# Kernel tuning notes

Hardware: AMD Instinct MI355X
Metric: run time of the kernel (lower is better)

The kernel has to match this reference:

```python
import jax, jax.numpy as jnp
import numpy as np

N = 50000       # num nodes
E = 800000      # num edges
F_NODE = 128    # input node feature dim
F_EDGE = 32     # input edge feature dim
H = 64          # hidden dim (heads=1)
NEG_SLOPE = 0.2 # GAT leaky-relu slope


def _segment_softmax(scores, seg, num_segments):
    # numerically stable softmax over edges grouped by destination node
    m = jax.ops.segment_max(scores, seg, num_segments=num_segments)
    ex = jnp.exp(scores - m[seg])
    denom = jax.ops.segment_sum(ex, seg, num_segments=num_segments)
    return ex / (denom[seg] + 1e-16)


def _egat_conv(x, src, dst, eattr, W, We, a_src, a_dst, a_e, b):
    # PyG-style GAT layer with edge features (heads=1, no self loops).
    xp = x @ W                      # [N, H] projected nodes
    ep = eattr @ We                 # [E, H] projected edges (returned as new edge feats)
    score = (xp @ a_src)[src] + (xp @ a_dst)[dst] + ep @ a_e  # [E]
    score = jax.nn.leaky_relu(score, NEG_SLOPE)
    alpha = _segment_softmax(score, dst, N)                    # [E]
    out = jax.ops.segment_sum(alpha[:, None] * xp[src], dst, num_segments=N) + b
    return out, alpha, ep


def setup_inputs() -> dict:
    key = jax.random.key(0)
    ks = jax.random.split(key, 24)
    inp = {
        "x": jax.random.normal(ks[0], (N, F_NODE), jnp.float32),
        "edge_index": jax.random.randint(ks[1], (2, E), 0, N, jnp.int64),
        "edge_attr": jax.random.normal(ks[2], (E, F_EDGE), jnp.float32),
    }
    def glorot(k, shape):
        fan = shape[0] + shape[-1]
        return jax.random.normal(k, shape, jnp.float32) * jnp.sqrt(2.0 / fan)
    dims = [(F_NODE, F_EDGE), (H, H), (H, H)]
    i = 3
    for li, (din, dedge) in enumerate(dims, start=1):
        inp[f"W{li}"] = glorot(ks[i], (din, H)); i += 1
        inp[f"We{li}"] = glorot(ks[i], (dedge, H)); i += 1
        inp[f"as{li}"] = glorot(ks[i], (H,)); i += 1
        inp[f"ad{li}"] = glorot(ks[i], (H,)); i += 1
        inp[f"ae{li}"] = glorot(ks[i], (H,)); i += 1
        inp[f"b{li}"] = jnp.zeros((H,), jnp.float32)
    inp["Wc"] = glorot(ks[i], (H, 1)); i += 1
    inp["bc"] = jnp.zeros((1,), jnp.float32)
    return inp


def reference(x, edge_index, edge_attr,
              W1, We1, as1, ad1, ae1, b1,
              W2, We2, as2, ad2, ae2, b2,
              W3, We3, as3, ad3, ae3, b3,
              Wc, bc):
    src, dst = edge_index[0], edge_index[1]
    # layer 1 (edge feats projected F_EDGE -> H, reused as next edge_attr)
    x1, _, e1 = _egat_conv(x, src, dst, edge_attr, W1, We1, as1, ad1, ae1, b1)
    x1 = jax.nn.relu(x1)  # dropout is identity in eval mode
    # layer 2
    x2, _, e2 = _egat_conv(x1, src, dst, e1, W2, We2, as2, ad2, ae2, b2)
    x2 = jax.nn.relu(x2)
    # layer 3
    x3, _, _ = _egat_conv(x2, src, dst, e2, W3, We3, as3, ad3, ae3, b3)
    x3 = jax.nn.relu(x3)
    return x3 @ Wc + bc  # [N, 1]
```

## Files before the change

kernel.cpp:

```cpp
#include <hip/hip_runtime.h>
#include <hip/hip_fp16.h>
#include <math.h>

#define NN 50000
#define NE 800000
#define FN 128
#define FE 32
#define HD 64
#define NB 49
#define GP ((NN + 127) / 128)
#define NT (NE / 64)
#define EB2 ((NT + 7) / 8)
#define GE ((NE + 255) / 256)

typedef unsigned long long u64;
typedef unsigned short u16;

__global__ void k_vecs_zero(const float* __restrict__ We1, const float* __restrict__ We2,
                            const float* __restrict__ We3, const float* __restrict__ ae1,
                            const float* __restrict__ ae2, const float* __restrict__ ae3,
                            float* __restrict__ v123, int* __restrict__ deg) {
  const int i = blockIdx.x * blockDim.x + threadIdx.x;
  if (i < NN) deg[i] = 0;
  if (blockIdx.x != 0) return;
  __shared__ float u2[HD], u3[HD], u23[HD];
  const int t = threadIdx.x;
  if (t < HD) {
    float s2 = 0.f, s3 = 0.f;
    for (int j = 0; j < HD; ++j) {
      s2 += We2[t * HD + j] * ae2[j];
      s3 += We3[t * HD + j] * ae3[j];
    }
    u2[t] = s2; u3[t] = s3;
  }
  __syncthreads();
  if (t < HD) {
    float s23 = 0.f;
    for (int j = 0; j < HD; ++j) s23 += We2[t * HD + j] * u3[j];
    u23[t] = s23;
  }
  __syncthreads();
  if (t < FE) {
    float a = 0.f, b = 0.f, c = 0.f;
    for (int j = 0; j < HD; ++j) {
      float w = We1[t * HD + j];
      a += w * ae1[j];
      b += w * u2[j];
      c += w * u23[j];
    }
    v123[t] = a; v123[32 + t] = b; v123[64 + t] = c;
  }
}

__global__ __launch_bounds__(256) void k_mega4(
    const float* __restrict__ x, const float* __restrict__ W,
    const float* __restrict__ asv, const float* __restrict__ adv,
    __half* __restrict__ xph, float* __restrict__ ssrc, float* __restrict__ sdst,
    const int* __restrict__ srcA, const int* __restrict__ dstA,
    const float* __restrict__ eattr, const float* __restrict__ v123,
    int* __restrict__ deg, u16* __restrict__ rank, u64* __restrict__ trec) {
  const int t = threadIdx.x;
  if (blockIdx.x >= GP) {
    const int kb = blockIdx.x - GP;
    const int w = t >> 6, lane = t & 63;
    const int g = lane >> 3, q = lane & 7;
    const float4 v1q = *(const float4*)(v123 + q * 4);
    const float4 v2q = *(const float4*)(v123 + 32 + q * 4);
    const float4 v3q = *(const float4*)(v123 + 64 + q * 4);
    const int perm = 8 * q + g;
#pragma unroll
    for (int it = 0; it < 2; ++it) {
      const int tIdx = kb * 8 + w * 2 + it;
      if (tIdx < NT) {
        const int E0 = tIdx * 64;
        const int e = E0 + perm;
        const int d = dstA[e];
        const int s = srcA[e];
        const int r = atomicAdd(&deg[d], 1);
        float ra = 0.f, rb = 0.f, rc = 0.f;
#pragma unroll
        for (int k = 0; k < 8; ++k) {
          const float4 xv =
              *(const float4*)(eattr + (size_t)(E0 + 8 * k + g) * FE + q * 4);
          float a = xv.x * v1q.x + xv.y * v1q.y + xv.z * v1q.z + xv.w * v1q.w;
          float b = xv.x * v2q.x + xv.y * v2q.y + xv.z * v2q.z + xv.w * v2q.w;
          float c = xv.x * v3q.x + xv.y * v3q.y + xv.z * v3q.z + xv.w * v3q.w;
#pragma unroll
          for (int off = 1; off < 8; off <<= 1) {
            a += __shfl_xor(a, off);
            b += __shfl_xor(b, off);
            c += __shfl_xor(c, off);
          }
          if (q == k) { ra = a; rb = b; rc = c; }
        }
        trec[e] = (u64)(u16)s
                | ((u64)__half_as_ushort(__float2half_rn(ra)) << 16)
                | ((u64)__half_as_ushort(__float2half_rn(rb)) << 32)
                | ((u64)__half_as_ushort(__float2half_rn(rc)) << 48);
        rank[e] = (u16)r;
      }
    }
    return;
  }
  const int w = t >> 6, l = t & 63;
  const int g = w * 4 + (l >> 4);
  const int rr = g * 8;
  const int c0 = (l & 15) * 4;
  const int row0 = blockIdx.x * 128;

  int xoff[8];
#pragma unroll
  for (int i = 0; i < 8; ++i) {
    int gr = row0 + rr + i;
    xoff[i] = (gr < NN ? gr : NN - 1) * FN;
  }

  float acc[8][4];
#pragma unroll
  for (int i = 0; i < 8; ++i)
#pragma unroll
    for (int j = 0; j < 4; ++j) acc[i][j] = 0.f;

  for (int k = 0; k < FN; k += 4) {
    float wv[4][4];
#pragma unroll
    for (int kk = 0; kk < 4; ++kk) {
      float4 wq = *(const float4*)(W + (k + kk) * HD + c0);
      wv[kk][0] = wq.x; wv[kk][1] = wq.y; wv[kk][2] = wq.z; wv[kk][3] = wq.w;
    }
#pragma unroll
    for (int i = 0; i < 8; ++i) {
      float4 a = *(const float4*)(x + xoff[i] + k);
#pragma unroll
      for (int j = 0; j < 4; ++j)
        acc[i][j] += a.x * wv[0][j] + a.y * wv[1][j] + a.z * wv[2][j] + a.w * wv[3][j];
    }
  }

  float as4[4], ad4[4];
#pragma unroll
  for (int j = 0; j < 4; ++j) { as4[j] = asv[c0 + j]; ad4[j] = adv[c0 + j]; }
#pragma unroll
  for (int i = 0; i < 8; ++i) {
    int gr = row0 + rr + i;
    float ps = 0.f, pd = 0.f;
#pragma unroll
    for (int j = 0; j < 4; ++j) {
      ps += acc[i][j] * as4[j];
      pd += acc[i][j] * ad4[j];
    }
#pragma unroll
    for (int off = 1; off < 16; off <<= 1) {
      ps += __shfl_xor(ps, off);
      pd += __shfl_xor(pd, off);
    }
    if (gr < NN) {
      union { __half2 h2[2]; float2 f2; } u;
      u.h2[0] = __floats2half2_rn(acc[i][0], acc[i][1]);
      u.h2[1] = __floats2half2_rn(acc[i][2], acc[i][3]);
      *(float2*)(xph + (size_t)gr * HD + c0) = u.f2;
      if ((l & 15) == 0) { ssrc[gr] = ps; sdst[gr] = pd; }
    }
  }
}

__global__ __launch_bounds__(256) void k_scanA(const int* __restrict__ deg,
                                               int* __restrict__ bsum) {
  __shared__ int ws[4];
  const int t = threadIdx.x, lane = t & 63, wid = t >> 6;
  const int i0 = blockIdx.x * 1024 + t * 4;
  int s = 0;
#pragma unroll
  for (int j = 0; j < 4; ++j) {
    int i = i0 + j;
    if (i < NN) s += deg[i];
  }
#pragma unroll
  for (int off = 32; off; off >>= 1) s += __shfl_xor(s, off);
  if (lane == 0) ws[wid] = s;
  __syncthreads();
  if (t == 0) bsum[blockIdx.x] = ws[0] + ws[1] + ws[2] + ws[3];
}

__global__ __launch_bounds__(256) void k_scanB(const int* __restrict__ deg,
                                               const int* __restrict__ bsum,
                                               int* __restrict__ row_ptr) {
  __shared__ int blockOff;
  __shared__ int wOff[4];
  const int b = blockIdx.x;
  const int t = threadIdx.x, lane = t & 63, wid = t >> 6;
  if (t < 64) {
    int v = (t < NB) ? bsum[t] : 0;
    int p = v;
#pragma unroll
    for (int off = 1; off < 64; off <<= 1) {
      int u = __shfl_up(p, off);
      if (lane >= off) p += u;
    }
    if (t == b) blockOff = p - v;
    if (b == 0 && t == NB - 1) row_ptr[NN] = p;
  }
  __syncthreads();
  const int i0 = b * 1024 + t * 4;
  int v[4];
#pragma unroll
  for (int j = 0; j < 4; ++j) {
    int i = i0 + j;
    v[j] = (i < NN) ? deg[i] : 0;
  }
  int s = v[0] + v[1] + v[2] + v[3];
  int p = s;
#pragma unroll
  for (int off = 1; off < 64; off <<= 1) {
    int u = __shfl_up(p, off);
    if (lane >= off) p += u;
  }
  if (lane == 63) wOff[wid] = p;
  __syncthreads();
  int woff = 0;
  for (int wq = 0; wq < wid; ++wq) woff += wOff[wq];
  int excl = blockOff + woff + (p - s);
#pragma unroll
  for (int j = 0; j < 4; ++j) {
    int i = i0 + j;
    if (i < NN) row_ptr[i] = excl;
    excl += v[j];
  }
}

__global__ void k_scatter(const int* __restrict__ dstA, const u16* __restrict__ rank,
                          const int* __restrict__ row_ptr, const u64* __restrict__ trec,
                          u64* __restrict__ aos) {
  const int e = blockIdx.x * blockDim.x + threadIdx.x;
  if (e >= NE) return;
  aos[row_ptr[dstA[e]] + (int)rank[e]] = trec[e];
}

template <int TSEL>
__global__ __launch_bounds__(256) void k_agg_proj(
    const int* __restrict__ row_ptr, const u64* __restrict__ aos,
    const __half* __restrict__ xin, const float* __restrict__ ssrc_in,
    const float* __restrict__ sdst_in, const float* __restrict__ bias,
    const float* __restrict__ Wn, const float* __restrict__ asn,
    const float* __restrict__ adn, __half* __restrict__ xout,
    float* __restrict__ ssrc_out, float* __restrict__ sdst_out) {
  __shared__ __half swh[HD * HD];
  const int t = threadIdx.x;
  for (int i = t; i < HD * HD; i += 256) swh[i] = __float2half_rn(Wn[i]);

  const int gw = (blockIdx.x * blockDim.x + t) >> 6;
  const int lane = t & 63;
  const int g = lane >> 3;
  const int q = lane & 7;
  const int n = gw * 8 + g;
  const bool act = n < NN;
  int beg = 0, end = 0;
  float sd = 0.f;
  if (act) { beg = row_ptr[n]; end = row_ptr[n + 1]; sd = sdst_in[n]; }

  float dsum = 0.f;
  float4 o0 = make_float4(0.f, 0.f, 0.f, 0.f);
  float4 o1 = make_float4(0.f, 0.f, 0.f, 0.f);
  for (int base = beg; base < end; base += 16) {
    const int p0 = base + q, p1 = base + 8 + q;
    float pe0 = 0.f, pe1 = 0.f;
    int s0 = 0, s1 = 0;
    if (p0 < end) {
      u64 r = aos[p0];
      s0 = (int)(r & 0xFFFFu);
      float tt = __half2float(__ushort_as_half((u16)((r >> (16 * TSEL)) & 0xFFFFu)));
      float raw = ssrc_in[s0] + sd + tt;
      raw = raw > 0.f ? raw : 0.2f * raw;
      pe0 = __expf(raw);
    }
    if (p1 < end) {
      u64 r = aos[p1];
      s1 = (int)(r & 0xFFFFu);
      float tt = __half2float(__ushort_as_half((u16)((r >> (16 * TSEL)) & 0xFFFFu)));
      float raw = ssrc_in[s1] + sd + tt;
      raw = raw > 0.f ? raw : 0.2f * raw;
      pe1 = __expf(raw);
    }
    dsum += pe0 + pe1;
#pragma unroll
    for (int j = 0; j < 8; ++j) {
      const int sl = g * 8 + j;
      float pa = __shfl(pe0, sl);
      int sa = __shfl(s0, sl);
      float pb = __shfl(pe1, sl);
      int sb = __shfl(s1, sl);
      union { float4 f4; __half2 h2[4]; } ua, ub;
      ua.f4 = ((const float4*)(xin + (size_t)sa * HD))[q];
      ub.f4 = ((const float4*)(xin + (size_t)sb * HD))[q];
      float2 a0 = __half22float2(ua.h2[0]);
      float2 a1 = __half22float2(ua.h2[1]);
      float2 a2 = __half22float2(ua.h2[2]);
      float2 a3 = __half22float2(ua.h2[3]);
      o0.x += pa * a0.x; o0.y += pa * a0.y; o0.z += pa * a1.x; o0.w += pa * a1.y;
      o1.x += pa * a2.x; o1.y += pa * a2.y; o1.z += pa * a3.x; o1.w += pa * a3.y;
      float2 b0 = __half22float2(ub.h2[0]);
      float2 b1 = __half22float2(ub.h2[1]);
      float2 b2 = __half22float2(ub.h2[2]);
      float2 b3 = __half22float2(ub.h2[3]);
      o0.x += pb * b0.x; o0.y += pb * b0.y; o0.z += pb * b1.x; o0.w += pb * b1.y;
      o1.x += pb * b2.x; o1.y += pb * b2.y; o1.z += pb * b3.x; o1.w += pb * b3.y;
    }
  }
#pragma unroll
  for (int off = 1; off < 8; off <<= 1) dsum += __shfl_xor(dsum, off);

  const float inv = 1.f / (dsum + 1e-16f);
  const float4 b0 = ((const float4*)bias)[q * 2];
  const float4 b1 = ((const float4*)bias)[q * 2 + 1];
  float vreg[8];
  vreg[0] = fmaxf(o0.x * inv + b0.x, 0.f);
  vreg[1] = fmaxf(o0.y * inv + b0.y, 0.f);
  vreg[2] = fmaxf(o0.z * inv + b0.z, 0.f);
  vreg[3] = fmaxf(o0.w * inv + b0.w, 0.f);
  vreg[4] = fmaxf(o1.x * inv + b1.x, 0.f);
  vreg[5] = fmaxf(o1.y * inv + b1.y, 0.f);
  vreg[6] = fmaxf(o1.z * inv + b1.z, 0.f);
  vreg[7] = fmaxf(o1.w * inv + b1.w, 0.f);

  __syncthreads();

  float out8[8] = {0.f, 0.f, 0.f, 0.f, 0.f, 0.f, 0.f, 0.f};
#pragma unroll
  for (int kq = 0; kq < 8; ++kq) {
#pragma unroll
    for (int m = 0; m < 8; ++m) {
      float vb = __shfl(vreg[m], (lane & 56) | kq);
      union { float4 f4; __half2 h2[4]; } uw;
      uw.f4 = *(const float4*)(swh + (kq * 8 + m) * HD + q * 8);
      float2 w0 = __half22float2(uw.h2[0]);
      float2 w1 = __half22float2(uw.h2[1]);
      float2 w2 = __half22float2(uw.h2[2]);
      float2 w3 = __half22float2(uw.h2[3]);
      out8[0] += vb * w0.x; out8[1] += vb * w0.y;
      out8[2] += vb * w1.x; out8[3] += vb * w1.y;
      out8[4] += vb * w2.x; out8[5] += vb * w2.y;
      out8[6] += vb * w3.x; out8[7] += vb * w3.y;
    }
  }

  float ps = 0.f, pd = 0.f;
#pragma unroll
  for (int j = 0; j < 8; ++j) {
    ps += out8[j] * asn[q * 8 + j];
    pd += out8[j] * adn[q * 8 + j];
  }
#pragma unroll
  for (int off = 1; off < 8; off <<= 1) {
    ps += __shfl_xor(ps, off);
    pd += __shfl_xor(pd, off);
  }

  if (!act) return;
  union { float4 f4; __half2 h2[4]; } wv;
  wv.h2[0] = __floats2half2_rn(out8[0], out8[1]);
  wv.h2[1] = __floats2half2_rn(out8[2], out8[3]);
  wv.h2[2] = __floats2half2_rn(out8[4], out8[5]);
  wv.h2[3] = __floats2half2_rn(out8[6], out8[7]);
  ((float4*)(xout + (size_t)n * HD))[q] = wv.f4;
  if (q == 0) { ssrc_out[n] = ps; sdst_out[n] = pd; }
}

template <int TSEL>
__global__ __launch_bounds__(256) void k_agg_head(
    const int* __restrict__ row_ptr, const u64* __restrict__ aos,
    const __half* __restrict__ xin, const float* __restrict__ ssrc_in,
    const float* __restrict__ sdst_in, const float* __restrict__ bias,
    const float* __restrict__ Wc, const float* __restrict__ bc,
    float* __restrict__ outf) {
  const int gw = (blockIdx.x * blockDim.x + threadIdx.x) >> 6;
  const int lane = threadIdx.x & 63;
  const int g = lane >> 3;
  const int q = lane & 7;
  const int n = gw * 8 + g;
  const bool act = n < NN;
  int beg = 0, end = 0;
  float sd = 0.f;
  if (act) { beg = row_ptr[n]; end = row_ptr[n + 1]; sd = sdst_in[n]; }

  float dsum = 0.f;
  float4 o0 = make_float4(0.f, 0.f, 0.f, 0.f);
  float4 o1 = make_float4(0.f, 0.f, 0.f, 0.f);
  for (int base = beg; base < end; base += 16) {
    const int p0 = base + q, p1 = base + 8 + q;
    float pe0 = 0.f, pe1 = 0.f;
    int s0 = 0, s1 = 0;
    if (p0 < end) {
      u64 r = aos[p0];
      s0 = (int)(r & 0xFFFFu);
      float tt = __half2float(__ushort_as_half((u16)((r >> (16 * TSEL)) & 0xFFFFu)));
      float raw = ssrc_in[s0] + sd + tt;
      raw = raw > 0.f ? raw : 0.2f * raw;
      pe0 = __expf(raw);
    }
    if (p1 < end) {
      u64 r = aos[p1];
      s1 = (int)(r & 0xFFFFu);
      float tt = __half2float(__ushort_as_half((u16)((r >> (16 * TSEL)) & 0xFFFFu)));
      float raw = ssrc_in[s1] + sd + tt;
      raw = raw > 0.f ? raw : 0.2f * raw;
      pe1 = __expf(raw);
    }
    dsum += pe0 + pe1;
#pragma unroll
    for (int j = 0; j < 8; ++j) {
      const int sl = g * 8 + j;
      float pa = __shfl(pe0, sl);
      int sa = __shfl(s0, sl);
      float pb = __shfl(pe1, sl);
      int sb = __shfl(s1, sl);
      union { float4 f4; __half2 h2[4]; } ua, ub;
      ua.f4 = ((const float4*)(xin + (size_t)sa * HD))[q];
      ub.f4 = ((const float4*)(xin + (size_t)sb * HD))[q];
      float2 a0 = __half22float2(ua.h2[0]);
      float2 a1 = __half22float2(ua.h2[1]);
      float2 a2 = __half22float2(ua.h2[2]);
      float2 a3 = __half22float2(ua.h2[3]);
      o0.x += pa * a0.x; o0.y += pa * a0.y; o0.z += pa * a1.x; o0.w += pa * a1.y;
      o1.x += pa * a2.x; o1.y += pa * a2.y; o1.z += pa * a3.x; o1.w += pa * a3.y;
      float2 b0 = __half22float2(ub.h2[0]);
      float2 b1 = __half22float2(ub.h2[1]);
      float2 b2 = __half22float2(ub.h2[2]);
      float2 b3 = __half22float2(ub.h2[3]);
      o0.x += pb * b0.x; o0.y += pb * b0.y; o0.z += pb * b1.x; o0.w += pb * b1.y;
      o1.x += pb * b2.x; o1.y += pb * b2.y; o1.z += pb * b3.x; o1.w += pb * b3.y;
    }
  }
#pragma unroll
  for (int off = 1; off < 8; off <<= 1) dsum += __shfl_xor(dsum, off);

  if (!act) return;
  const float inv = 1.f / (dsum + 1e-16f);
  const float4 b0 = ((const float4*)bias)[q * 2];
  const float4 b1 = ((const float4*)bias)[q * 2 + 1];
  const float4 w0 = ((const float4*)Wc)[q * 2];
  const float4 w1 = ((const float4*)Wc)[q * 2 + 1];
  float c = fmaxf(o0.x * inv + b0.x, 0.f) * w0.x +
            fmaxf(o0.y * inv + b0.y, 0.f) * w0.y +
            fmaxf(o0.z * inv + b0.z, 0.f) * w0.z +
            fmaxf(o0.w * inv + b0.w, 0.f) * w0.w +
            fmaxf(o1.x * inv + b1.x, 0.f) * w1.x +
            fmaxf(o1.y * inv + b1.y, 0.f) * w1.y +
            fmaxf(o1.z * inv + b1.z, 0.f) * w1.z +
            fmaxf(o1.w * inv + b1.w, 0.f) * w1.w;
#pragma unroll
  for (int off = 1; off < 8; off <<= 1) c += __shfl_xor(c, off);
  if (q == 0) outf[n] = c + bc[0];
}

extern "C" void kernel_launch(void* const* d_in, const int* in_sizes, int n_in,
                              void* d_out, int out_size, void* d_ws, size_t ws_size,
                              hipStream_t stream) {
  const float* x     = (const float*)d_in[0];
  const int*   ei    = (const int*)d_in[1];
  const float* eattr = (const float*)d_in[2];
  const float* W1  = (const float*)d_in[3];
  const float* We1 = (const float*)d_in[4];
  const float* as1 = (const float*)d_in[5];
  const float* ad1 = (const float*)d_in[6];
  const float* ae1 = (const float*)d_in[7];
  const float* b1  = (const float*)d_in[8];
  const float* W2  = (const float*)d_in[9];
  const float* We2 = (const float*)d_in[10];
  const float* as2 = (const float*)d_in[11];
  const float* ad2 = (const float*)d_in[12];
  const float* ae2 = (const float*)d_in[13];
  const float* b2  = (const float*)d_in[14];
  const float* W3  = (const float*)d_in[15];
  const float* We3 = (const float*)d_in[16];
  const float* as3 = (const float*)d_in[17];
  const float* ad3 = (const float*)d_in[18];
  const float* ae3 = (const float*)d_in[19];
  const float* b3  = (const float*)d_in[20];
  const float* Wc  = (const float*)d_in[21];
  const float* bc  = (const float*)d_in[22];

  const int* srcA = ei;
  const int* dstA = ei + NE;
  float* outf = (float*)d_out;

  char* w = (char*)d_ws;
  auto alloc = [&](size_t bytes) {
    char* p = w;
    w += (bytes + 255) & ~(size_t)255;
    return p;
  };
  float* v123 = (float*)alloc(96 * 4);
  u64* aos = (u64*)alloc((size_t)NE * 8);
  u64* trec = (u64*)alloc((size_t)NE * 8);
  u16* rank = (u16*)alloc((size_t)NE * 2);
  int* row_ptr = (int*)alloc((size_t)(NN + 1) * 4);
  int* deg = (int*)alloc((size_t)NN * 4);
  int* bsum = (int*)alloc((size_t)NB * 4);
  __half* xpA = (__half*)alloc((size_t)NN * HD * 2);
  __half* xpB = (__half*)alloc((size_t)NN * HD * 2);
  float* ssrcA = (float*)alloc((size_t)NN * 4);
  float* sdstA = (float*)alloc((size_t)NN * 4);
  float* ssrcB = (float*)alloc((size_t)NN * 4);
  float* sdstB = (float*)alloc((size_t)NN * 4);

  const int gN = (NN + 255) / 256;
  const int gA = ((NN + 7) / 8 * 64 + 255) / 256;

  k_vecs_zero<<<gN, 256, 0, stream>>>(We1, We2, We3, ae1, ae2, ae3, v123, deg);
  k_mega4<<<GP + EB2, 256, 0, stream>>>(x, W1, as1, ad1, xpA, ssrcA, sdstA,
                                        srcA, dstA, eattr, v123, deg, rank, trec);
  k_scanA<<<NB, 256, 0, stream>>>(deg, bsum);
  k_scanB<<<NB, 256, 0, stream>>>(deg, bsum, row_ptr);
  k_scatter<<<GE, 256, 0, stream>>>(dstA, rank, row_ptr, trec, aos);
  k_agg_proj<1><<<gA, 256, 0, stream>>>(row_ptr, aos, xpA, ssrcA, sdstA, b1,
                                        W2, as2, ad2, xpB, ssrcB, sdstB);
  k_agg_proj<2><<<gA, 256, 0, stream>>>(row_ptr, aos, xpB, ssrcB, sdstB, b2,
                                        W3, as3, ad3, xpA, ssrcA, sdstA);
  k_agg_head<3><<<gA, 256, 0, stream>>>(row_ptr, aos, xpA, ssrcA, sdstA, b3,
                                        Wc, bc, outf);
}
```

Baseline: 151.8 us.

## Stage edge attributes into LDS via direct global-to-LDS loads in edge blocks

The edge branch of the fused first kernel now loads 1024 edges per block. It issues their 32-float attribute rows straight into shared memory with global_load_lds, and each thread then computes its edge's three dot products from LDS with a rotated index to spread bank accesses. This replaces the earlier per-lane float4 loads followed by xor-shuffle reductions. The atomic degree counting is batched up front for the block's four 256-edge chunks. The cost is a 32 KB shared buffer declared for every block, including the node-projection blocks, which may lower occupancy for the GEMM part, plus two barriers per chunk.

```diff
diff --git a/kernel.cpp b/kernel.cpp
--- a/kernel.cpp
+++ b/kernel.cpp
@@ -9,12 +9,13 @@
 #define HD 64
 #define NB 49
 #define GP ((NN + 127) / 128)
-#define NT (NE / 64)
-#define EB2 ((NT + 7) / 8)
+#define EB3 ((NE + 1023) / 1024)
 #define GE ((NE + 255) / 256)
 
 typedef unsigned long long u64;
 typedef unsigned short u16;
+typedef const void __attribute__((address_space(1)))* gas_t;
+typedef void __attribute__((address_space(3)))* las_t;
 
 __global__ void k_vecs_zero(const float* __restrict__ We1, const float* __restrict__ We2,
                             const float* __restrict__ We3, const float* __restrict__ ae1,
@@ -52,53 +53,71 @@
   }
 }
 
-__global__ __launch_bounds__(256) void k_mega4(
+__global__ __launch_bounds__(256) void k_mega7(
     const float* __restrict__ x, const float* __restrict__ W,
     const float* __restrict__ asv, const float* __restrict__ adv,
     __half* __restrict__ xph, float* __restrict__ ssrc, float* __restrict__ sdst,
     const int* __restrict__ srcA, const int* __restrict__ dstA,
     const float* __restrict__ eattr, const float* __restrict__ v123,
     int* __restrict__ deg, u16* __restrict__ rank, u64* __restrict__ trec) {
+  __shared__ float sbuf[8192];
+  __shared__ float sv[96];
   const int t = threadIdx.x;
   if (blockIdx.x >= GP) {
     const int kb = blockIdx.x - GP;
+    const int base = kb * 1024;
     const int w = t >> 6, lane = t & 63;
-    const int g = lane >> 3, q = lane & 7;
-    const float4 v1q = *(const float4*)(v123 + q * 4);
-    const float4 v2q = *(const float4*)(v123 + 32 + q * 4);
-    const float4 v3q = *(const float4*)(v123 + 64 + q * 4);
-    const int perm = 8 * q + g;
-#pragma unroll
-    for (int it = 0; it < 2; ++it) {
-      const int tIdx = kb * 8 + w * 2 + it;
-      if (tIdx < NT) {
-        const int E0 = tIdx * 64;
-        const int e = E0 + perm;
+    if (t < 96) sv[t] = v123[t];
+
+    int sE[4], rE[4];
+#pragma unroll
+    for (int c = 0; c < 4; ++c) {
+      const int e = base + c * 256 + t;
+      sE[c] = 0; rE[c] = 0;
+      if (e < NE) {
         const int d = dstA[e];
-        const int s = srcA[e];
-        const int r = atomicAdd(&deg[d], 1);
-        float ra = 0.f, rb = 0.f, rc = 0.f;
-#pragma unroll
-        for (int k = 0; k < 8; ++k) {
-          const float4 xv =
-              *(const float4*)(eattr + (size_t)(E0 + 8 * k + g) * FE + q * 4);
-          float a = xv.x * v1q.x + xv.y * v1q.y + xv.z * v1q.z + xv.w * v1q.w;
-          float b = xv.x * v2q.x + xv.y * v2q.y + xv.z * v2q.z + xv.w * v2q.w;
-          float c = xv.x * v3q.x + xv.y * v3q.y + xv.z * v3q.z + xv.w * v3q.w;
-#pragma unroll
-          for (int off = 1; off < 8; off <<= 1) {
-            a += __shfl_xor(a, off);
-            b += __shfl_xor(b, off);
-            c += __shfl_xor(c, off);
-          }
-          if (q == k) { ra = a; rb = b; rc = c; }
+        sE[c] = srcA[e];
+        rE[c] = atomicAdd(&deg[d], 1);
+      }
+    }
+
+    const int jrot = t & 7;
+#pragma unroll 1
+    for (int c = 0; c < 4; ++c) {
+      const bool cv = (base + c * 256) < NE;
+      if (cv) {
+        const size_t gf = (size_t)(base + c * 256) * FE;
+#pragma unroll
+        for (int i = 0; i < 8; ++i) {
+          const int seg = w * 8 + i;
+          const float* g = eattr + gf + seg * 256 + lane * 4;
+          __builtin_amdgcn_global_load_lds((gas_t)g, (las_t)(sbuf + seg * 256),
+                                           16, 0, 0);
         }
-        trec[e] = (u64)(u16)s
-                | ((u64)__half_as_ushort(__float2half_rn(ra)) << 16)
-                | ((u64)__half_as_ushort(__float2half_rn(rb)) << 32)
-                | ((u64)__half_as_ushort(__float2half_rn(rc)) << 48);
-        rank[e] = (u16)r;
       }
+      __syncthreads();
+      if (cv) {
+        const float* row = sbuf + (t << 5);
+        float a = 0.f, b = 0.f, cc = 0.f;
+#pragma unroll
+        for (int j = 0; j < 8; ++j) {
+          const int jj = j ^ jrot;
+          const float4 xv = *(const float4*)(row + jj * 4);
+          const float4 w1 = *(const float4*)(sv + jj * 4);
+          const float4 w2 = *(const float4*)(sv + 32 + jj * 4);
+          const float4 w3 = *(const float4*)(sv + 64 + jj * 4);
+          a  += xv.x * w1.x + xv.y * w1.y + xv.z * w1.z + xv.w * w1.w;
+          b  += xv.x * w2.x + xv.y * w2.y + xv.z * w2.z + xv.w * w2.w;
+          cc += xv.x * w3.x + xv.y * w3.y + xv.z * w3.z + xv.w * w3.w;
+        }
+        const int e = base + c * 256 + t;
+        trec[e] = (u64)(u16)sE[c]
+                | ((u64)__half_as_ushort(__float2half_rn(a)) << 16)
+                | ((u64)__half_as_ushort(__float2half_rn(b)) << 32)
+                | ((u64)__half_as_ushort(__float2half_rn(cc)) << 48);
+        rank[e] = (u16)rE[c];
+      }
+      __syncthreads();
     }
     return;
   }
@@ -507,7 +526,7 @@
   const int gA = ((NN + 7) / 8 * 64 + 255) / 256;
 
   k_vecs_zero<<<gN, 256, 0, stream>>>(We1, We2, We3, ae1, ae2, ae3, v123, deg);
-  k_mega4<<<GP + EB2, 256, 0, stream>>>(x, W1, as1, ad1, xpA, ssrcA, sdstA,
+  k_mega7<<<GP + EB3, 256, 0, stream>>>(x, W1, as1, ad1, xpA, ssrcA, sdstA,
                                         srcA, dstA, eattr, v123, deg, rank, trec);
   k_scanA<<<NB, 256, 0, stream>>>(deg, bsum);
   k_scanB<<<NB, 256, 0, stream>>>(deg, bsum, row_ptr);
```

Measured after the change: 164.4 us. 8.3% more time.
